# Performance work log

Hardware: AMD Instinct MI355X
Metric: run time of the kernel (lower is better)

Reference implementation:

```python
import jax, jax.numpy as jnp
import numpy as np

# Forest of complete L-ary trees, BFS level-contiguous node numbering.
B_TREES, ARITY, DEPTH = 8, 4, 8
C, M, NGEN = 8, 100, 4
COUNTS = [B_TREES * ARITY**l for l in range(DEPTH + 1)]
OFFS = np.concatenate([[0], np.cumsum(COUNTS)]).astype(np.int64)
DIM = int(OFFS[-1])  # 699048
# tree id of each node: within-level index // (ARITY**level)
BATCH = np.concatenate([np.arange(COUNTS[l]) // (ARITY**l) for l in range(DEPTH + 1)])


def setup_inputs() -> dict:
    key = jax.random.key(0)
    k1, k2, k3, k4 = jax.random.split(key, 4)
    return {
        "x": jax.random.randint(k1, (DIM,), 0, M, dtype=jnp.int32),
        "A": jax.random.normal(k2, (C, C, ARITY, NGEN), dtype=jnp.float32) * 2.5,
        "B_emit": jax.random.normal(k3, (C, M, NGEN), dtype=jnp.float32) * 2.5,
        "Pi": jax.random.normal(k4, (C, NGEN), dtype=jnp.float32) * 2.5,
    }


def _htmm_loglik(x, A, B_emit, Pi):
    # softmax reparameterization (matches F.softmax axes in torch code)
    smA = jax.nn.softmax(A, axis=0)            # [C,C,L,G], over child state
    smA_t = jnp.transpose(smA, (2, 0, 1, 3))   # [L,C,C,G]
    smB = jax.nn.softmax(B_emit, axis=1)       # [C,M,G]
    smPi = jax.nn.softmax(Pi, axis=0)          # [C,G]

    # preliminary downward: prior state distribution per node, level by level.
    # Children of a parent are contiguous with sibling position j = idx % ARITY.
    prior_lvls = [jnp.broadcast_to(smPi, (COUNTS[0], C, NGEN))]
    for l in range(1, DEPTH + 1):
        n_pa = COUNTS[l - 1]
        # prior_child[c] = sum_d A[c, d, pos_j, g] * prior_pa[d]
        pl = jnp.einsum('jcdg,pdg->pjcg', smA_t, prior_lvls[-1])
        prior_lvls.append(pl.reshape(n_pa * ARITY, C, NGEN))
    prior = jnp.concatenate(prior_lvls, axis=0)  # [DIM,C,G]

    em = jnp.transpose(smB[:, x], (1, 0, 2))     # [DIM,C,G]
    beta0 = prior * em

    ll = jnp.zeros((DIM, NGEN), dtype=beta0.dtype)
    # leaves = deepest level
    beta_lvl = beta0[OFFS[DEPTH]:OFFS[DEPTH + 1]]
    nu = beta_lvl.sum(1)                          # [n_leaves,G]
    beta_lvl = beta_lvl / nu[:, None, :]
    ll = ll.at[OFFS[DEPTH]:OFFS[DEPTH + 1]].set(jnp.log(nu))

    # upward recursion, bottom-up
    for l in range(DEPTH, 0, -1):
        n_pa = COUNTS[l - 1]
        ratio = (beta_lvl / prior[OFFS[l]:OFFS[l + 1]]).reshape(n_pa, ARITY, C, NGEN)
        # beta_uv[d] = sum_c A[c, d, pos_j, g] * beta_ch[c] / prior_ch[c]
        beta_uv = jnp.einsum('jcdg,pjcg->pjdg', smA_t, ratio)  # [n_pa,L,C,G]
        beta_pa = beta0[OFFS[l - 1]:OFFS[l]] * jnp.prod(beta_uv, axis=1)
        nu = beta_pa.sum(1)
        beta_lvl = beta_pa / nu[:, None, :]
        ll = ll.at[OFFS[l - 1]:OFFS[l]].set(jnp.log(nu))

    # scatter per-node log-likelihood contributions into per-tree totals
    return jax.ops.segment_sum(ll, jnp.asarray(BATCH), num_segments=B_TREES)  # [B_TREES,G]


def reference(x, A, B_emit, Pi):
    return _htmm_loglik(x, A, B_emit, Pi)
```

## Files before the change

### kernel.cpp

```cpp
#include <hip/hip_runtime.h>

constexpr int OFFS1 = 8, OFFS2 = 40, OFFS3 = 168, OFFS4 = 680;
constexpr int OFFS5 = 2728, OFFS6 = 10920, OFFS7 = 43688, OFFS8 = 174760;


#define WB() __builtin_amdgcn_wave_barrier()
#define AG_ST(p, v) __hip_atomic_store((p), (v), __ATOMIC_RELAXED, __HIP_MEMORY_SCOPE_AGENT)
#define AG_LD(p) __hip_atomic_load((p), __ATOMIC_RELAXED, __HIP_MEMORY_SCOPE_AGENT)

template <int CTRL>
static __device__ __forceinline__ float dppmov(float v) {
  return __int_as_float(__builtin_amdgcn_update_dpp(0, __float_as_int(v), CTRL, 0xF, 0xF, true));
}
static __device__ __forceinline__ float bfly8(float v) {
  v += dppmov<0xB1>(v);
  v += dppmov<0x4E>(v);
  v += dppmov<0x141>(v);
  return v;
}
static __device__ __forceinline__ float red16(float v) {
  v += dppmov<0xB1>(v);
  v += dppmov<0x4E>(v);
  v += dppmov<0x141>(v);
  v += dppmov<0x140>(v);
  return v;
}
constexpr int PX[8] = {0, 1, 2, 3, 7, 6, 5, 4};
struct O8 { float a[8]; };
static __device__ __forceinline__ O8 gather8(float v) {
  O8 o;
  o.a[0] = v;
  o.a[1] = dppmov<0xB1>(v);
  o.a[2] = dppmov<0x4E>(v);
  o.a[3] = dppmov<0x1B>(v);
  o.a[4] = dppmov<0x141>(v);
  o.a[5] = dppmov<0x141>(o.a[1]);
  o.a[6] = dppmov<0x141>(o.a[2]);
  o.a[7] = dppmov<0x141>(o.a[3]);
  return o;
}
static __device__ __forceinline__ float mvc(const float w[8], const O8& o) {
  float acc = 0.f;
#pragma unroll
  for (int i = 0; i < 8; i++) acc += w[i] * o.a[i];
  return acc;
}
static __device__ __forceinline__ float mv_sel(const float wq[4][8], const O8& o, int j) {
  float acc = 0.f;
#pragma unroll
  for (int i = 0; i < 8; i++) {
    float w01 = (j & 1) ? wq[1][i] : wq[0][i];
    float w23 = (j & 1) ? wq[3][i] : wq[2][i];
    float w = (j & 2) ? w23 : w01;
    acc += w * o.a[i];
  }
  return acc;
}
static __device__ __forceinline__ float dot8r(const float w[8], const float* p) {
  const float4* q = (const float4*)p;
  float4 a = q[0], b = q[1];
  return w[0] * a.x + w[1] * a.y + w[2] * a.z + w[3] * a.w +
         w[4] * b.x + w[5] * b.y + w[6] * b.z + w[7] * b.w;
}
static __device__ __forceinline__ void ld8(const float* p, float pv[8]) {
  const float4* q = (const float4*)p;
  float4 a = q[0], b = q[1];
  pv[0] = a.x; pv[1] = a.y; pv[2] = a.z; pv[3] = a.w;
  pv[4] = b.x; pv[5] = b.y; pv[6] = b.z; pv[7] = b.w;
}
static __device__ __forceinline__ float rcpf(float x) { return __builtin_amdgcn_rcpf(x); }

constexpr int SMEM_F = 19936;

__global__ __launch_bounds__(512) void k_all(const int* __restrict__ x,
                                             const float* __restrict__ A,
                                             const float* __restrict__ Bm,
                                             const float* __restrict__ Pi,
                                             float* __restrict__ RAT4,
                                             float* __restrict__ blocksum,
                                             unsigned* __restrict__ ctr,
                                             float* __restrict__ out) {
  __shared__ __align__(16) float smem[SMEM_F];
  __shared__ float llb[4];
  __shared__ int lastf;
  float* wtd_l = smem;
  float* pit_l = smem + 1024;
  float* stash = smem + 1056;
  float* rat5buf = smem + 3104;
  float* pri4buf = smem + 3616;
  float* emt_f = smem + 3744;
  float* rat4_l = smem + 3744;
  _Float16* emt_h = (_Float16*)(smem + 11936);
  _Float16* etab_h = (_Float16*)(smem + 13536);

  int t = threadIdx.x;
  int r = t & 31, g = r >> 3, s = r & 7, grp = t >> 5;
  int b = blockIdx.x, tree = b >> 6;

  if (t < 128) {
    int d = t >> 4, j = (t >> 2) & 3, gg = t & 3;
    float v[8], sum = 0.f;
#pragma unroll
    for (int ss = 0; ss < 8; ss++) { v[ss] = __expf(A[((ss * 8 + d) * 4 + j) * 4 + gg]); sum += v[ss]; }
    float inv = rcpf(sum);
#pragma unroll
    for (int ss = 0; ss < 8; ss++) wtd_l[(j * 8 + d) * 32 + gg * 8 + ss] = v[ss] * inv;
  }
  if (t < 4) {
    float v[8], sum = 0.f;
#pragma unroll
    for (int c = 0; c < 8; c++) { v[c] = __expf(Pi[c * 4 + t]); sum += v[c]; }
    float inv = rcpf(sum);
#pragma unroll
    for (int c = 0; c < 8; c++) pit_l[t * 8 + c] = v[c] * inv;
    llb[t] = 0.f;
  }
  {
    int row = t >> 4, part = t & 15, c = row >> 2, gg = row & 3;
    int m0 = part < 4 ? part * 7 : 28 + (part - 4) * 6;
    int mn = part < 4 ? 7 : 6;
    float sum = 0.f;
    for (int m = m0; m < m0 + mn; m++) sum += __expf(Bm[(c * 100 + m) * 4 + gg]);
    sum = red16(sum);
    float inv = rcpf(sum);
    for (int m = m0; m < m0 + mn; m++) {
      float e = __expf(Bm[(c * 100 + m) * 4 + gg]) * inv;
      emt_f[m * 32 + gg * 8 + c] = e;
      emt_h[m * 32 + gg * 8 + c] = (_Float16)e;
    }
  }
  __syncthreads();
  {
    int j = grp & 3, mq = grp >> 2;
    float wu8[8];
#pragma unroll
    for (int i = 0; i < 8; i++) wu8[i] = wtd_l[(j * 8 + s) * 32 + g * 8 + (s ^ PX[i])];
    for (int m = mq * 25; m < mq * 25 + 25; m++) {
      O8 o = gather8(emt_f[m * 32 + r]);
      etab_h[(m * 4 + j) * 32 + r] = (_Float16)mvc(wu8, o);
    }
  }
  float wq[4][8], wup_r[4][8];
#pragma unroll
  for (int j = 0; j < 4; j++) {
#pragma unroll
    for (int i = 0; i < 8; i++) wq[j][i] = wtd_l[(j * 8 + (s ^ PX[i])) * 32 + r];
    ld8(&wtd_l[(j * 8 + s) * 32 + g * 8], wup_r[j]);
  }
  __syncthreads();

  float* st = stash + grp * 128;
  int n5 = b * 16 + grp;
  float acc = 0.f;

  float v = pit_l[r], pri4 = 0.f;
#pragma unroll
  for (int k = 1; k <= 5; k++) {
    O8 o = gather8(v);
    int j = (n5 >> (2 * (5 - k))) & 3;
    v = mv_sel(wq, o, j);
    if (k == 4) pri4 = v;
  }
  float v5 = v;
  O8 o5 = gather8(v5);

  const int4* x8v = (const int4*)(x + OFFS8 + n5 * 64);
  const int4* x7v = (const int4*)(x + OFFS7 + n5 * 16);
  int4 x6v = *(const int4*)(x + OFFS6 + n5 * 4);
  int x5s = x[OFFS5 + n5];
  const int* x6a = (const int*)&x6v;

  float l6r[4];
#pragma unroll
  for (int q6 = 0; q6 < 4; q6++) {
    int4 x7 = x7v[q6];
    const int* x7a = (const int*)&x7;
    float u6 = mvc(wq[q6], o5);
    O8 o6 = gather8(u6);
    float Ep[4][4];
#pragma unroll
    for (int q7 = 0; q7 < 4; q7++) {
      int4 xl = x8v[q6 * 4 + q7];
      const int* xla = (const int*)&xl;
#pragma unroll
      for (int j = 0; j < 4; j++) Ep[q7][j] = (float)etab_h[(xla[j] * 4 + j) * 32 + r];
    }
#pragma unroll
    for (int q7 = 0; q7 < 4; q7++) {
      float u7 = mvc(wq[q7], o6);
      float n0 = bfly8(u7 * Ep[q7][0]);
      float n1 = bfly8(u7 * Ep[q7][1]);
      float n2 = bfly8(u7 * Ep[q7][2]);
      float n3 = bfly8(u7 * Ep[q7][3]);
      float p01 = n0 * n1, p23 = n2 * n3;
      float prod = (Ep[q7][0] * Ep[q7][1] * rcpf(p01)) * (Ep[q7][2] * Ep[q7][3] * rcpf(p23));
      acc += __logf(p01) + __logf(p23);
      float em = (float)emt_h[x7a[q7] * 32 + r];
      float nu7 = bfly8(u7 * em * prod);
      acc += __logf(nu7);
      st[q7 * 32 + r] = em * prod * rcpf(nu7);
    }
    WB();
    float prod6 = 1.f;
#pragma unroll
    for (int j = 0; j < 4; j++) prod6 *= dot8r(wup_r[j], st + j * 32 + g * 8);
    WB();
    float em6 = (float)emt_h[x6a[q6] * 32 + r];
    float nu6 = bfly8(u6 * em6 * prod6);
    acc += __logf(nu6);
    l6r[q6] = em6 * prod6 * rcpf(nu6);
  }
#pragma unroll
  for (int j = 0; j < 4; j++) st[j * 32 + r] = l6r[j];
  WB();
  {
    float prod5 = 1.f;
#pragma unroll
    for (int j = 0; j < 4; j++) prod5 *= dot8r(wup_r[j], st + j * 32 + g * 8);
    float em5 = (float)emt_h[x5s * 32 + r];
    float nu5 = bfly8(v5 * em5 * prod5);
    acc += __logf(nu5);
    rat5buf[grp * 32 + r] = em5 * prod5 * rcpf(nu5);
  }
  if ((grp & 3) == 0) pri4buf[(grp >> 2) * 32 + r] = pri4;
  __syncthreads();

  if (grp < 4) {
    int n4 = b * 4 + grp;
    float prod = 1.f;
#pragma unroll
    for (int j = 0; j < 4; j++) prod *= dot8r(wup_r[j], &rat5buf[(grp * 4 + j) * 32 + g * 8]);
    float em = (float)emt_h[x[OFFS4 + n4] * 32 + r];
    float nu = bfly8(pri4buf[grp * 32 + r] * em * prod);
    acc += __logf(nu);
    AG_ST(&RAT4[n4 * 32 + r], em * prod * rcpf(nu));
  }

  if (s == 0) atomicAdd(&llb[g], acc);
  __syncthreads();
  if (t < 4) AG_ST(&blocksum[b * 4 + t], llb[t]);
  asm volatile("s_waitcnt vmcnt(0)" ::: "memory");
  __syncthreads();
  if (t == 0) {
    unsigned old = __hip_atomic_fetch_add(&ctr[tree * 32], 1u, __ATOMIC_RELAXED,
                                          __HIP_MEMORY_SCOPE_AGENT);
    lastf = (old == 63u || old == 0xAAAAAAE9u) ? 1 : 0;
  }
  __syncthreads();
  if (!lastf) return;

  if (t < 4) llb[t] = 0.f;
  {
    float tmp[16];
#pragma unroll
    for (int i = 0; i < 16; i++) tmp[i] = AG_LD(&RAT4[tree * 8192 + i * 512 + t]);
#pragma unroll
    for (int i = 0; i < 16; i++) rat4_l[i * 512 + t] = tmp[i];
  }
  __syncthreads();

  float acc2 = 0.f;
  {
    int n2g = tree * 16 + grp;
    float v2 = pit_l[r];
#pragma unroll
    for (int k = 1; k <= 2; k++) {
      O8 o = gather8(v2);
      int j = (n2g >> (2 * (2 - k))) & 3;
      v2 = mv_sel(wq, o, j);
    }
    O8 o2 = gather8(v2);
#pragma unroll
    for (int j3 = 0; j3 < 4; j3++) {
      int n3g = n2g * 4 + j3;
      int i3l = grp * 4 + j3;
      float p3 = mvc(wq[j3], o2);
      float prod = 1.f;
#pragma unroll
      for (int j = 0; j < 4; j++) prod *= dot8r(wup_r[j], &rat4_l[(i3l * 4 + j) * 32 + g * 8]);
      float em = (float)emt_h[x[OFFS3 + n3g] * 32 + r];
      float nu = bfly8(p3 * em * prod);
      acc2 += __logf(nu);
      st[j3 * 32 + r] = em * prod * rcpf(nu);
    }
    WB();
    float prod = 1.f;
#pragma unroll
    for (int j = 0; j < 4; j++) prod *= dot8r(wup_r[j], st + j * 32 + g * 8);
    WB();
    float em = (float)emt_h[x[OFFS2 + n2g] * 32 + r];
    float nu = bfly8(v2 * em * prod);
    acc2 += __logf(nu);
    rat5buf[grp * 32 + r] = em * prod * rcpf(nu);
  }
  __syncthreads();
  if (grp < 4) {
    int n1g = tree * 4 + grp;
    O8 op = gather8(pit_l[r]);
    float v1 = mv_sel(wq, op, grp);
    float prod = 1.f;
#pragma unroll
    for (int j = 0; j < 4; j++) prod *= dot8r(wup_r[j], &rat5buf[(grp * 4 + j) * 32 + g * 8]);
    float em = (float)emt_h[x[OFFS1 + n1g] * 32 + r];
    float nu = bfly8(v1 * em * prod);
    acc2 += __logf(nu);
    pri4buf[grp * 32 + r] = em * prod * rcpf(nu);
  }
  __syncthreads();
  if (grp == 0) {
    float prod = 1.f;
#pragma unroll
    for (int j = 0; j < 4; j++) prod *= dot8r(wup_r[j], &pri4buf[j * 32 + g * 8]);
    float em = (float)emt_h[x[tree] * 32 + r];
    float nu = bfly8(pit_l[r] * em * prod);
    acc2 += __logf(nu);
  }
  if (s == 0) atomicAdd(&llb[g], acc2);
  __syncthreads();
  float* red = rat4_l;
  if (t < 256) red[t] = AG_LD(&blocksum[tree * 256 + t]);
  __syncthreads();
#pragma unroll
  for (int off = 128; off >= 4; off >>= 1) {
    if (t < off) red[t] += red[t + off];
    __syncthreads();
  }
  if (t < 4) out[tree * 4 + t] = red[t] + llb[t];
}

extern "C" void kernel_launch(void* const* d_in, const int* in_sizes, int n_in,
                              void* d_out, int out_size, void* d_ws, size_t ws_size,
                              hipStream_t stream) {
  const int* x = (const int*)d_in[0];
  const float* A = (const float*)d_in[1];
  const float* Bm = (const float*)d_in[2];
  const float* Pi = (const float*)d_in[3];
  float* ws = (float*)d_ws;
  unsigned* ctr = (unsigned*)d_ws;
  float* blocksum = ws + 256;
  float* RAT4 = ws + 256 + 2048;
  float* out = (float*)d_out;

  k_all<<<512, 512, 0, stream>>>(x, A, Bm, Pi, RAT4, blocksum, ctr, out);
}
```

Baseline: 108.0 us.

## Halve block size, replace LDS stash matvecs with DPP transposed matvec, shrink LDS

Blocks drop from 512 to 256 threads, and each wave handles two subtrees in a loop. The upward matvec that went through an LDS stash and wave barriers is replaced by a DPP-based transposed matvec (mvup) that reuses the wq registers. This removes the wup_r registers and the stash traffic. Pi softmax is computed per lane in registers, and the final-block RAT4 staging is stored as fp16 to shrink LDS from about 80KB to about 49KB, allowing two blocks per CU. The trade-offs are extra DPP ops, fp16 precision loss on level-4 ratios, and serialized rounds per wave.

```diff
diff --git a/kernel.cpp b/kernel.cpp
--- a/kernel.cpp
+++ b/kernel.cpp
@@ -4,7 +4,6 @@
 constexpr int OFFS5 = 2728, OFFS6 = 10920, OFFS7 = 43688, OFFS8 = 174760;
 
 
-#define WB() __builtin_amdgcn_wave_barrier()
 #define AG_ST(p, v) __hip_atomic_store((p), (v), __ATOMIC_RELAXED, __HIP_MEMORY_SCOPE_AGENT)
 #define AG_LD(p) __hip_atomic_load((p), __ATOMIC_RELAXED, __HIP_MEMORY_SCOPE_AGENT)
 
@@ -16,13 +15,6 @@
   v += dppmov<0xB1>(v);
   v += dppmov<0x4E>(v);
   v += dppmov<0x141>(v);
-  return v;
-}
-static __device__ __forceinline__ float red16(float v) {
-  v += dppmov<0xB1>(v);
-  v += dppmov<0x4E>(v);
-  v += dppmov<0x141>(v);
-  v += dppmov<0x140>(v);
   return v;
 }
 constexpr int PX[8] = {0, 1, 2, 3, 7, 6, 5, 4};
@@ -56,45 +48,41 @@
   }
   return acc;
 }
-static __device__ __forceinline__ float dot8r(const float w[8], const float* p) {
-  const float4* q = (const float4*)p;
-  float4 a = q[0], b = q[1];
-  return w[0] * a.x + w[1] * a.y + w[2] * a.z + w[3] * a.w +
-         w[4] * b.x + w[5] * b.y + w[6] * b.z + w[7] * b.w;
-}
-static __device__ __forceinline__ void ld8(const float* p, float pv[8]) {
-  const float4* q = (const float4*)p;
-  float4 a = q[0], b = q[1];
-  pv[0] = a.x; pv[1] = a.y; pv[2] = a.z; pv[3] = a.w;
-  pv[4] = b.x; pv[5] = b.y; pv[6] = b.z; pv[7] = b.w;
+static __device__ __forceinline__ float mvup(const float w[8], float ratio) {
+  float inA = w[0] * ratio;
+  inA += dppmov<0xB1>(w[1] * ratio);
+  inA += dppmov<0x4E>(w[2] * ratio);
+  inA += dppmov<0x1B>(w[3] * ratio);
+  float inB = w[4] * ratio;
+  inB += dppmov<0xB1>(w[5] * ratio);
+  inB += dppmov<0x4E>(w[6] * ratio);
+  inB += dppmov<0x1B>(w[7] * ratio);
+  return inA + dppmov<0x141>(inB);
 }
 static __device__ __forceinline__ float rcpf(float x) { return __builtin_amdgcn_rcpf(x); }
 
-constexpr int SMEM_F = 19936;
-
-__global__ __launch_bounds__(512) void k_all(const int* __restrict__ x,
-                                             const float* __restrict__ A,
-                                             const float* __restrict__ Bm,
-                                             const float* __restrict__ Pi,
-                                             float* __restrict__ RAT4,
-                                             float* __restrict__ blocksum,
-                                             unsigned* __restrict__ ctr,
-                                             float* __restrict__ out) {
-  __shared__ __align__(16) float smem[SMEM_F];
+__global__ __launch_bounds__(256, 2) void k_all(const int* __restrict__ x,
+                                                const float* __restrict__ A,
+                                                const float* __restrict__ Bm,
+                                                const float* __restrict__ Pi,
+                                                float* __restrict__ RAT4,
+                                                float* __restrict__ blocksum,
+                                                unsigned* __restrict__ ctr,
+                                                float* __restrict__ out) {
+  __shared__ __align__(16) float smem[12320];
   __shared__ float llb[4];
   __shared__ int lastf;
   float* wtd_l = smem;
-  float* pit_l = smem + 1024;
-  float* stash = smem + 1056;
-  float* rat5buf = smem + 3104;
-  float* pri4buf = smem + 3616;
-  float* emt_f = smem + 3744;
-  float* rat4_l = smem + 3744;
-  _Float16* emt_h = (_Float16*)(smem + 11936);
-  _Float16* etab_h = (_Float16*)(smem + 13536);
-
-  int t = threadIdx.x;
-  int r = t & 31, g = r >> 3, s = r & 7, grp = t >> 5;
+  float* rat5buf = smem;
+  float* pri4buf = smem + 512;
+  float* rat2buf = smem;
+  float* rat1buf = smem + 512;
+  float* emt_f = smem + 1024;
+  _Float16* rat4h = (_Float16*)(smem + 1024);
+  _Float16* emt_h = (_Float16*)(smem + 5120);
+  _Float16* etab_h = (_Float16*)(smem + 5920);
+
+  int t = threadIdx.x, r = t & 31, g = r >> 3, s = r & 7, grp = t >> 5;
   int b = blockIdx.x, tree = b >> 6;
 
   if (t < 128) {
@@ -106,22 +94,14 @@
 #pragma unroll
     for (int ss = 0; ss < 8; ss++) wtd_l[(j * 8 + d) * 32 + gg * 8 + ss] = v[ss] * inv;
   }
-  if (t < 4) {
-    float v[8], sum = 0.f;
-#pragma unroll
-    for (int c = 0; c < 8; c++) { v[c] = __expf(Pi[c * 4 + t]); sum += v[c]; }
-    float inv = rcpf(sum);
-#pragma unroll
-    for (int c = 0; c < 8; c++) pit_l[t * 8 + c] = v[c] * inv;
-    llb[t] = 0.f;
-  }
+  if (t < 4) llb[t] = 0.f;
   {
-    int row = t >> 4, part = t & 15, c = row >> 2, gg = row & 3;
-    int m0 = part < 4 ? part * 7 : 28 + (part - 4) * 6;
-    int mn = part < 4 ? 7 : 6;
+    int row = t >> 3, part = t & 7, c = row >> 2, gg = row & 3;
+    int m0 = part < 4 ? part * 13 : 52 + (part - 4) * 12;
+    int mn = part < 4 ? 13 : 12;
     float sum = 0.f;
     for (int m = m0; m < m0 + mn; m++) sum += __expf(Bm[(c * 100 + m) * 4 + gg]);
-    sum = red16(sum);
+    sum = bfly8(sum);
     float inv = rcpf(sum);
     for (int m = m0; m < m0 + mn; m++) {
       float e = __expf(Bm[(c * 100 + m) * 4 + gg]) * inv;
@@ -129,107 +109,111 @@
       emt_h[m * 32 + gg * 8 + c] = (_Float16)e;
     }
   }
-  __syncthreads();
+  float pit_r;
   {
-    int j = grp & 3, mq = grp >> 2;
-    float wu8[8];
-#pragma unroll
-    for (int i = 0; i < 8; i++) wu8[i] = wtd_l[(j * 8 + s) * 32 + g * 8 + (s ^ PX[i])];
-    for (int m = mq * 25; m < mq * 25 + 25; m++) {
-      O8 o = gather8(emt_f[m * 32 + r]);
-      etab_h[(m * 4 + j) * 32 + r] = (_Float16)mvc(wu8, o);
-    }
-  }
-  float wq[4][8], wup_r[4][8];
-#pragma unroll
-  for (int j = 0; j < 4; j++) {
+    float sum = 0.f, own = 0.f;
+#pragma unroll
+    for (int c = 0; c < 8; c++) {
+      float e = __expf(Pi[c * 4 + g]);
+      sum += e;
+      if (c == s) own = e;
+    }
+    pit_r = own * rcpf(sum);
+  }
+  __syncthreads();
+  float wq[4][8];
+#pragma unroll
+  for (int j = 0; j < 4; j++)
 #pragma unroll
     for (int i = 0; i < 8; i++) wq[j][i] = wtd_l[(j * 8 + (s ^ PX[i])) * 32 + r];
-    ld8(&wtd_l[(j * 8 + s) * 32 + g * 8], wup_r[j]);
-  }
-  __syncthreads();
-
-  float* st = stash + grp * 128;
-  int n5 = b * 16 + grp;
+  {
+    int j = grp & 3, half = grp >> 2;
+    float wsel[8];
+#pragma unroll
+    for (int i = 0; i < 8; i++) {
+      float w01 = (j & 1) ? wq[1][i] : wq[0][i];
+      float w23 = (j & 1) ? wq[3][i] : wq[2][i];
+      wsel[i] = (j & 2) ? w23 : w01;
+    }
+    for (int m = half * 50; m < half * 50 + 50; m++)
+      etab_h[(m * 4 + j) * 32 + r] = (_Float16)mvup(wsel, emt_f[m * 32 + r]);
+  }
+  __syncthreads();
+
   float acc = 0.f;
-
-  float v = pit_l[r], pri4 = 0.f;
-#pragma unroll
-  for (int k = 1; k <= 5; k++) {
-    O8 o = gather8(v);
-    int j = (n5 >> (2 * (5 - k))) & 3;
-    v = mv_sel(wq, o, j);
-    if (k == 4) pri4 = v;
-  }
-  float v5 = v;
-  O8 o5 = gather8(v5);
-
-  const int4* x8v = (const int4*)(x + OFFS8 + n5 * 64);
-  const int4* x7v = (const int4*)(x + OFFS7 + n5 * 16);
-  int4 x6v = *(const int4*)(x + OFFS6 + n5 * 4);
-  int x5s = x[OFFS5 + n5];
-  const int* x6a = (const int*)&x6v;
-
-  float l6r[4];
-#pragma unroll
-  for (int q6 = 0; q6 < 4; q6++) {
-    int4 x7 = x7v[q6];
-    const int* x7a = (const int*)&x7;
-    float u6 = mvc(wq[q6], o5);
-    O8 o6 = gather8(u6);
-    float Ep[4][4];
-#pragma unroll
-    for (int q7 = 0; q7 < 4; q7++) {
-      int4 xl = x8v[q6 * 4 + q7];
-      const int* xla = (const int*)&xl;
-#pragma unroll
-      for (int j = 0; j < 4; j++) Ep[q7][j] = (float)etab_h[(xla[j] * 4 + j) * 32 + r];
-    }
-#pragma unroll
-    for (int q7 = 0; q7 < 4; q7++) {
-      float u7 = mvc(wq[q7], o6);
-      float n0 = bfly8(u7 * Ep[q7][0]);
-      float n1 = bfly8(u7 * Ep[q7][1]);
-      float n2 = bfly8(u7 * Ep[q7][2]);
-      float n3 = bfly8(u7 * Ep[q7][3]);
-      float p01 = n0 * n1, p23 = n2 * n3;
-      float prod = (Ep[q7][0] * Ep[q7][1] * rcpf(p01)) * (Ep[q7][2] * Ep[q7][3] * rcpf(p23));
-      acc += __logf(p01) + __logf(p23);
-      float em = (float)emt_h[x7a[q7] * 32 + r];
-      float nu7 = bfly8(u7 * em * prod);
-      acc += __logf(nu7);
-      st[q7 * 32 + r] = em * prod * rcpf(nu7);
-    }
-    WB();
-    float prod6 = 1.f;
-#pragma unroll
-    for (int j = 0; j < 4; j++) prod6 *= dot8r(wup_r[j], st + j * 32 + g * 8);
-    WB();
-    float em6 = (float)emt_h[x6a[q6] * 32 + r];
-    float nu6 = bfly8(u6 * em6 * prod6);
-    acc += __logf(nu6);
-    l6r[q6] = em6 * prod6 * rcpf(nu6);
-  }
-#pragma unroll
-  for (int j = 0; j < 4; j++) st[j * 32 + r] = l6r[j];
-  WB();
-  {
-    float prod5 = 1.f;
-#pragma unroll
-    for (int j = 0; j < 4; j++) prod5 *= dot8r(wup_r[j], st + j * 32 + g * 8);
+#pragma unroll 1
+  for (int round = 0; round < 2; round++) {
+    int n5 = b * 16 + round * 8 + grp;
+    float v = pit_r, pri4 = 0.f;
+#pragma unroll
+    for (int k = 1; k <= 5; k++) {
+      O8 o = gather8(v);
+      int j = (n5 >> (2 * (5 - k))) & 3;
+      v = mv_sel(wq, o, j);
+      if (k == 4) pri4 = v;
+    }
+    float v5 = v;
+    O8 o5 = gather8(v5);
+
+    const int4* x8v = (const int4*)(x + OFFS8 + n5 * 64);
+    const int4* x7v = (const int4*)(x + OFFS7 + n5 * 16);
+    int4 x6v = *(const int4*)(x + OFFS6 + n5 * 4);
+    int x5s = x[OFFS5 + n5];
+    const int* x6a = (const int*)&x6v;
+
+    float l6r[4];
+#pragma unroll
+    for (int q6 = 0; q6 < 4; q6++) {
+      int4 x7 = x7v[q6];
+      const int* x7a = (const int*)&x7;
+      float u6 = mvc(wq[q6], o5);
+      O8 o6 = gather8(u6);
+      float Ep[4][4];
+#pragma unroll
+      for (int q7 = 0; q7 < 4; q7++) {
+        int4 xl = x8v[q6 * 4 + q7];
+        const int* xla = (const int*)&xl;
+#pragma unroll
+        for (int j = 0; j < 4; j++) Ep[q7][j] = (float)etab_h[(xla[j] * 4 + j) * 32 + r];
+      }
+      float rat7[4];
+#pragma unroll
+      for (int q7 = 0; q7 < 4; q7++) {
+        float u7 = mvc(wq[q7], o6);
+        float n0 = bfly8(u7 * Ep[q7][0]);
+        float n1 = bfly8(u7 * Ep[q7][1]);
+        float n2 = bfly8(u7 * Ep[q7][2]);
+        float n3 = bfly8(u7 * Ep[q7][3]);
+        float p01 = n0 * n1, p23 = n2 * n3;
+        float prodL = (Ep[q7][0] * Ep[q7][1] * rcpf(p01)) * (Ep[q7][2] * Ep[q7][3] * rcpf(p23));
+        float em = (float)emt_h[x7a[q7] * 32 + r];
+        float nu7 = bfly8(u7 * em * prodL);
+        acc += __logf(p01 * p23) + __logf(nu7);
+        rat7[q7] = em * prodL * rcpf(nu7);
+      }
+      float prod6 = mvup(wq[0], rat7[0]) * mvup(wq[1], rat7[1]) *
+                    mvup(wq[2], rat7[2]) * mvup(wq[3], rat7[3]);
+      float em6 = (float)emt_h[x6a[q6] * 32 + r];
+      float nu6 = bfly8(u6 * em6 * prod6);
+      acc += __logf(nu6);
+      l6r[q6] = em6 * prod6 * rcpf(nu6);
+    }
+    float prod5 = mvup(wq[0], l6r[0]) * mvup(wq[1], l6r[1]) *
+                  mvup(wq[2], l6r[2]) * mvup(wq[3], l6r[3]);
     float em5 = (float)emt_h[x5s * 32 + r];
     float nu5 = bfly8(v5 * em5 * prod5);
     acc += __logf(nu5);
-    rat5buf[grp * 32 + r] = em5 * prod5 * rcpf(nu5);
-  }
-  if ((grp & 3) == 0) pri4buf[(grp >> 2) * 32 + r] = pri4;
+    rat5buf[(round * 8 + grp) * 32 + r] = em5 * prod5 * rcpf(nu5);
+    if ((grp & 3) == 0) pri4buf[(round * 2 + (grp >> 2)) * 32 + r] = pri4;
+  }
   __syncthreads();
 
   if (grp < 4) {
     int n4 = b * 4 + grp;
-    float prod = 1.f;
-#pragma unroll
-    for (int j = 0; j < 4; j++) prod *= dot8r(wup_r[j], &rat5buf[(grp * 4 + j) * 32 + g * 8]);
+    float prod = mvup(wq[0], rat5buf[(grp * 4 + 0) * 32 + r]) *
+                 mvup(wq[1], rat5buf[(grp * 4 + 1) * 32 + r]) *
+                 mvup(wq[2], rat5buf[(grp * 4 + 2) * 32 + r]) *
+                 mvup(wq[3], rat5buf[(grp * 4 + 3) * 32 + r]);
     float em = (float)emt_h[x[OFFS4 + n4] * 32 + r];
     float nu = bfly8(pri4buf[grp * 32 + r] * em * prod);
     acc += __logf(nu);
@@ -249,20 +233,25 @@
   __syncthreads();
   if (!lastf) return;
 
+  {
+    float tmp[8];
+#pragma unroll
+    for (int ib = 0; ib < 4; ib++) {
+#pragma unroll
+      for (int i = 0; i < 8; i++) tmp[i] = AG_LD(&RAT4[tree * 8192 + (ib * 8 + i) * 256 + t]);
+#pragma unroll
+      for (int i = 0; i < 8; i++) rat4h[(ib * 8 + i) * 256 + t] = (_Float16)tmp[i];
+    }
+  }
   if (t < 4) llb[t] = 0.f;
-  {
-    float tmp[16];
-#pragma unroll
-    for (int i = 0; i < 16; i++) tmp[i] = AG_LD(&RAT4[tree * 8192 + i * 512 + t]);
-#pragma unroll
-    for (int i = 0; i < 16; i++) rat4_l[i * 512 + t] = tmp[i];
-  }
   __syncthreads();
 
   float acc2 = 0.f;
-  {
-    int n2g = tree * 16 + grp;
-    float v2 = pit_l[r];
+#pragma unroll 1
+  for (int ii = 0; ii < 2; ii++) {
+    int l2 = ii * 8 + grp;
+    int n2g = tree * 16 + l2;
+    float v2 = pit_r;
 #pragma unroll
     for (int k = 1; k <= 2; k++) {
       O8 o = gather8(v2);
@@ -270,55 +259,51 @@
       v2 = mv_sel(wq, o, j);
     }
     O8 o2 = gather8(v2);
+    float rat3[4];
 #pragma unroll
     for (int j3 = 0; j3 < 4; j3++) {
-      int n3g = n2g * 4 + j3;
-      int i3l = grp * 4 + j3;
+      int i3l = l2 * 4 + j3;
       float p3 = mvc(wq[j3], o2);
-      float prod = 1.f;
-#pragma unroll
-      for (int j = 0; j < 4; j++) prod *= dot8r(wup_r[j], &rat4_l[(i3l * 4 + j) * 32 + g * 8]);
-      float em = (float)emt_h[x[OFFS3 + n3g] * 32 + r];
+      float prod = mvup(wq[0], (float)rat4h[(i3l * 4 + 0) * 32 + r]) *
+                   mvup(wq[1], (float)rat4h[(i3l * 4 + 1) * 32 + r]) *
+                   mvup(wq[2], (float)rat4h[(i3l * 4 + 2) * 32 + r]) *
+                   mvup(wq[3], (float)rat4h[(i3l * 4 + 3) * 32 + r]);
+      float em = (float)emt_h[x[OFFS3 + tree * 64 + i3l] * 32 + r];
       float nu = bfly8(p3 * em * prod);
       acc2 += __logf(nu);
-      st[j3 * 32 + r] = em * prod * rcpf(nu);
-    }
-    WB();
-    float prod = 1.f;
-#pragma unroll
-    for (int j = 0; j < 4; j++) prod *= dot8r(wup_r[j], st + j * 32 + g * 8);
-    WB();
-    float em = (float)emt_h[x[OFFS2 + n2g] * 32 + r];
-    float nu = bfly8(v2 * em * prod);
-    acc2 += __logf(nu);
-    rat5buf[grp * 32 + r] = em * prod * rcpf(nu);
+      rat3[j3] = em * prod * rcpf(nu);
+    }
+    float prod2 = mvup(wq[0], rat3[0]) * mvup(wq[1], rat3[1]) *
+                  mvup(wq[2], rat3[2]) * mvup(wq[3], rat3[3]);
+    float em2 = (float)emt_h[x[OFFS2 + n2g] * 32 + r];
+    float nu2 = bfly8(v2 * em2 * prod2);
+    acc2 += __logf(nu2);
+    rat2buf[l2 * 32 + r] = em2 * prod2 * rcpf(nu2);
   }
   __syncthreads();
   if (grp < 4) {
-    int n1g = tree * 4 + grp;
-    O8 op = gather8(pit_l[r]);
-    float v1 = mv_sel(wq, op, grp);
-    float prod = 1.f;
-#pragma unroll
-    for (int j = 0; j < 4; j++) prod *= dot8r(wup_r[j], &rat5buf[(grp * 4 + j) * 32 + g * 8]);
-    float em = (float)emt_h[x[OFFS1 + n1g] * 32 + r];
+    float v1 = mv_sel(wq, gather8(pit_r), grp);
+    float prod = mvup(wq[0], rat2buf[(grp * 4 + 0) * 32 + r]) *
+                 mvup(wq[1], rat2buf[(grp * 4 + 1) * 32 + r]) *
+                 mvup(wq[2], rat2buf[(grp * 4 + 2) * 32 + r]) *
+                 mvup(wq[3], rat2buf[(grp * 4 + 3) * 32 + r]);
+    float em = (float)emt_h[x[OFFS1 + tree * 4 + grp] * 32 + r];
     float nu = bfly8(v1 * em * prod);
     acc2 += __logf(nu);
-    pri4buf[grp * 32 + r] = em * prod * rcpf(nu);
+    rat1buf[grp * 32 + r] = em * prod * rcpf(nu);
   }
   __syncthreads();
   if (grp == 0) {
-    float prod = 1.f;
-#pragma unroll
-    for (int j = 0; j < 4; j++) prod *= dot8r(wup_r[j], &pri4buf[j * 32 + g * 8]);
+    float prod = mvup(wq[0], rat1buf[0 * 32 + r]) * mvup(wq[1], rat1buf[1 * 32 + r]) *
+                 mvup(wq[2], rat1buf[2 * 32 + r]) * mvup(wq[3], rat1buf[3 * 32 + r]);
     float em = (float)emt_h[x[tree] * 32 + r];
-    float nu = bfly8(pit_l[r] * em * prod);
+    float nu = bfly8(pit_r * em * prod);
     acc2 += __logf(nu);
   }
   if (s == 0) atomicAdd(&llb[g], acc2);
   __syncthreads();
-  float* red = rat4_l;
-  if (t < 256) red[t] = AG_LD(&blocksum[tree * 256 + t]);
+  float* red = smem + 1024;
+  red[t] = AG_LD(&blocksum[tree * 256 + t]);
   __syncthreads();
 #pragma unroll
   for (int off = 128; off >= 4; off >>= 1) {
@@ -341,5 +326,5 @@
   float* RAT4 = ws + 256 + 2048;
   float* out = (float*)d_out;
 
-  k_all<<<512, 512, 0, stream>>>(x, A, Bm, Pi, RAT4, blocksum, ctr, out);
-}
+  k_all<<<512, 256, 0, stream>>>(x, A, Bm, Pi, RAT4, blocksum, ctr, out);
+}
```

Result: faster. 98.15 us (-9.1%).
